# Kernel tuning notes

Hardware: AMD Instinct MI355X
Metric: run time of the kernel (lower is better)

The kernel has to match this reference:

```python
import jax, jax.numpy as jnp
import numpy as np

BN_EPS = 1e-5
L2_EPS = 1e-12


def setup_inputs() -> dict:
    key = jax.random.key(0)
    ks = jax.random.split(key, 4)
    B, C, H, W = 16, 384, 56, 56
    x = jax.random.normal(ks[0], (B, C, H, W), dtype=jnp.float32)
    w_qkv = jax.random.normal(ks[1], (3 * C, C), dtype=jnp.float32) * (1.0 / np.sqrt(C))
    b_qkv = jnp.zeros((3 * C,), dtype=jnp.float32)
    w_proj = jax.random.normal(ks[2], (C, C), dtype=jnp.float32) * (1.0 / np.sqrt(C))
    b_proj = jnp.zeros((C,), dtype=jnp.float32)
    bn_gamma = jnp.ones((C,), dtype=jnp.float32)
    bn_beta = jnp.zeros((C,), dtype=jnp.float32)
    bn_mean = jnp.zeros((C,), dtype=jnp.float32)
    bn_var = jnp.ones((C,), dtype=jnp.float32)
    temperature = jnp.ones((1,), dtype=jnp.float32)
    return {"x": x, "w_qkv": w_qkv, "b_qkv": b_qkv, "w_proj": w_proj,
            "b_proj": b_proj, "bn_gamma": bn_gamma, "bn_beta": bn_beta,
            "bn_mean": bn_mean, "bn_var": bn_var, "temperature": temperature}


def _l2norm_lastdim(t):
    # F.normalize(t, dim=-1): divide by max(||t||_2, eps)
    n = jnp.sqrt(jnp.sum(t * t, axis=-1, keepdims=True))
    return t / jnp.maximum(n, L2_EPS)


def reference(x, w_qkv, b_qkv, w_proj, b_proj, bn_gamma, bn_beta, bn_mean, bn_var, temperature):
    B, C, H, W = x.shape
    N = H * W
    # BatchNorm2d (eval mode, running stats)
    scale = bn_gamma / jnp.sqrt(bn_var + BN_EPS)          # [C]
    shift = bn_beta - bn_mean * scale                     # [C]
    xn = x * scale[None, :, None, None] + shift[None, :, None, None]
    # 1x1 conv qkv: C -> 3C, operate on flattened spatial [B, C, N]
    xn_f = xn.reshape(B, C, N)
    qkv = jnp.einsum('oc,bcn->bon', w_qkv, xn_f) + b_qkv[None, :, None]  # [B,3C,N]
    q, k, v = qkv[:, :C], qkv[:, C:2 * C], qkv[:, 2 * C:]
    q = _l2norm_lastdim(q)                                # [B,C,N]
    k = _l2norm_lastdim(k)
    # channel-transposed attention: [B,C,C]
    logits = jnp.einsum('bcn,bdn->bcd', q, k) * temperature[0]
    attn = jax.nn.softmax(logits, axis=-1)
    fused = jnp.einsum('bcd,bdn->bcn', attn, v)           # [B,C,N]
    # 1x1 proj conv + residual
    out = jnp.einsum('oc,bcn->bon', w_proj, fused) + b_proj[None, :, None]
    return x + out.reshape(B, C, H, W)
```

## Files before the change

### kernel.cpp

```cpp
#include <hip/hip_runtime.h>

#define BATCH 16
#define CCH   384
#define NSP   3136
#define NSPP  3200

typedef unsigned short u16;
typedef float  f32x4  __attribute__((ext_vector_type(4)));
typedef __bf16 bf16x8 __attribute__((ext_vector_type(8)));

__device__ __forceinline__ float bf2f(u16 u) {
  union { unsigned int i; float f; } v; v.i = ((unsigned int)u) << 16; return v.f;
}
__device__ __forceinline__ u16 f2bf(float f) {
  union { float f; unsigned int i; } v; v.f = f;
  unsigned int i = v.i;
  return (u16)((i + 0x7fffu + ((i >> 16) & 1u)) >> 16);
}
__device__ __forceinline__ float rdf(const void* p, long i, bool bf) {
  return bf ? bf2f(((const u16*)p)[i]) : ((const float*)p)[i];
}

__device__ __forceinline__ void gload_lds16(const u16* g, u16* l) {
  __builtin_amdgcn_global_load_lds(
      (const __attribute__((address_space(1))) void*)g,
      (__attribute__((address_space(3))) void*)l, 16, 0, 0);
}

__global__ void transpose_kernel(const void* __restrict__ x, u16* __restrict__ xt,
                                 u16* __restrict__ xbf, const u16* __restrict__ probe) {
  const bool bf = (probe[0] == 0x3F80u);
  __shared__ float Ls[32 * 65];
  const int t = threadIdx.x;
  const int n0 = blockIdx.x * 64, c0 = blockIdx.y * 32, b = blockIdx.z;
  if (n0 >= NSP) {
    const int n_l = t >> 2, c8 = (t & 3) * 8;
    uint4 zq = make_uint4(0, 0, 0, 0);
    *(uint4*)(xt + ((long)b * NSPP + n0 + n_l) * CCH + c0 + c8) = zq;
    return;
  }
  {
    const int c_l = t >> 3, n8 = (t & 7) * 8;
    const long src = ((long)b * CCH + c0 + c_l) * NSP + n0 + n8;
    float v[8];
    if (bf) {
      union { uint4 q; u16 e[8]; } u; u.q = *(const uint4*)((const u16*)x + src);
      #pragma unroll
      for (int i = 0; i < 8; i++) v[i] = bf2f(u.e[i]);
    } else {
      float4 a = *(const float4*)((const float*)x + src);
      float4 c = *(const float4*)((const float*)x + src + 4);
      v[0]=a.x; v[1]=a.y; v[2]=a.z; v[3]=a.w; v[4]=c.x; v[5]=c.y; v[6]=c.z; v[7]=c.w;
    }
    union { uint4 q; u16 e[8]; } ob;
    #pragma unroll
    for (int i = 0; i < 8; i++) { ob.e[i] = f2bf(v[i]); Ls[c_l * 65 + n8 + i] = v[i]; }
    *(uint4*)(xbf + src) = ob.q;
  }
  __syncthreads();
  {
    const int n_l = t >> 2, c8 = (t & 3) * 8;
    union { uint4 q; u16 e[8]; } o;
    #pragma unroll
    for (int i = 0; i < 8; i++) o.e[i] = f2bf(Ls[(c8 + i) * 65 + n_l]);
    *(uint4*)(xt + ((long)b * NSPP + n0 + n_l) * CCH + c0 + c8) = o.q;
  }
}

__global__ void prep_kernel(const void* __restrict__ w_qkv, const void* __restrict__ b_qkv,
                            const void* __restrict__ gamma, const void* __restrict__ beta,
                            const void* __restrict__ mean,  const void* __restrict__ var,
                            const void* __restrict__ b_proj, const void* __restrict__ w_proj,
                            u16* __restrict__ w_eff, float* __restrict__ b_eff,
                            float* __restrict__ bproj_f,
                            unsigned* __restrict__ w2qk, unsigned* __restrict__ wp2,
                            u16* __restrict__ wvT, float* __restrict__ szero,
                            const u16* __restrict__ probe) {
  const bool bf = (probe[0] == 0x3F80u);
  __shared__ float s_scale[CCH], s_shift[CCH];
  const int tid = threadIdx.x;
  const int o = blockIdx.x;
  if (o < 72) {
    szero[o * 256 + tid] = 0.f;
    szero[o * 256 + 128 + tid] = 0.f;
  }
  for (int c = tid; c < CCH; c += 128) {
    float g = rdf(gamma, c, bf), bt = rdf(beta, c, bf);
    float mn = rdf(mean, c, bf), vr = rdf(var, c, bf);
    float sc = g * rsqrtf(vr + 1e-5f);
    s_scale[c] = sc; s_shift[c] = bt - mn * sc;
  }
  __syncthreads();
  float part = 0.f;
  for (int c = tid; c < CCH; c += 128) {
    float w = rdf(w_qkv, (long)o * CCH + c, bf);
    u16 wv = f2bf(w * s_scale[c]);
    w_eff[(long)o * CCH + c] = wv;
    if (o < 768) w2qk[(long)o * CCH + c] = (unsigned)wv | ((unsigned)wv << 16);
    else         wvT[(long)c * CCH + (o - 768)] = wv;
    part += w * s_shift[c];
  }
  for (int off = 32; off > 0; off >>= 1) part += __shfl_down(part, off, 64);
  __shared__ float s_part[2];
  if ((tid & 63) == 0) s_part[tid >> 6] = part;
  __syncthreads();
  if (tid == 0) b_eff[o] = rdf(b_qkv, o, bf) + s_part[0] + s_part[1];
  if (o < CCH) {
    for (int c = tid; c < CCH; c += 128) {
      u16 pv = f2bf(rdf(w_proj, (long)o * CCH + c, bf));
      wp2[(long)o * CCH + c] = (unsigned)pv | ((unsigned)pv << 16);
    }
  }
  if (o == 0) {
    for (int c = tid; c < CCH; c += 128) bproj_f[c] = rdf(b_proj, c, bf);
  }
}

template<int BM, int BN, int WGM, int WGN, int OUTM, bool BIASM, bool RES,
         int NCHK, bool EPIL, bool SUMX, bool SYMM>
__launch_bounds__(256)
__global__ void gemm_nt(const u16* __restrict__ A, const u16* __restrict__ B,
                        void* __restrict__ Cv,
                        const float* __restrict__ biasm,
                        const void* __restrict__ resv,
                        int K, int lda, int ldb, int ldc,
                        long sA, long sB, long sC, long sRes,
                        int zb, int nLim, int sBM,
                        float* __restrict__ qns, const u16* __restrict__ epW,
                        float* __restrict__ sxp,
                        const u16* __restrict__ probe) {
  constexpr int WM = BM / WGM, WN = BN / WGN;
  constexpr int FM = WM / 16,  FN = WN / 16;
  constexpr int NA = BM / 32,  NB = BN / 32;
  constexpr bool BOUNCE = (OUTM == 1 || OUTM == 2) && (BM == BN) && (WGN == 2);
  constexpr int RPF = WGM * 16;
  constexpr int LBS = BN + 4;
  constexpr int SM_STAGE  = (BM + BN) * 128;
  constexpr int SM_BOUNCE = BOUNCE ? RPF * LBS * 4 : 0;
  constexpr int SM_BYTES  = SM_STAGE > SM_BOUNCE ? SM_STAGE : SM_BOUNCE;
  __shared__ __align__(16) char smem[SM_BYTES];
  u16* As = (u16*)smem;
  u16* Bs = (u16*)(smem + BM * 128);
  const bool f32io = (probe[0] != 0x3F80u);
  const int tid = threadIdx.x, wave = tid >> 6, lane = tid & 63;
  const int quad = lane >> 4, l16 = lane & 15;
  const int wm = wave / WGN, wn = wave % WGN;
  const int z = blockIdx.z;
  A += z * sA; B += z * sB;
  const long cOff = (long)(zb + z) * sC;
  const long rOff = (long)(zb + z) * sRes;

  const int gx = gridDim.x;
  const int tot = gx * gridDim.y;
  const int wg = blockIdx.y * gx + blockIdx.x;
  const int qq = tot >> 3, rr = tot & 7;
  const int xcd = wg & 7, idx = wg >> 3;
  const int nid = (xcd < rr ? xcd * (qq + 1) : rr * (qq + 1) + (xcd - rr) * qq) + idx;
  const int m0 = (nid % gx) * BM, n0 = (nid / gx) * BN;
  if (SYMM && n0 > m0) return;

  const u16* ag[NA];
  const u16* bg[NB];
  #pragma unroll
  for (int p = 0; p < NA; p++) {
    int u = tid + p * 256, r = u >> 3, k8 = u & 7;
    ag[p] = A + (long)(m0 + r) * lda + ((k8 ^ (r & 7)) << 3);
  }
  #pragma unroll
  for (int p = 0; p < NB; p++) {
    int u = tid + p * 256, r = u >> 3, k8 = u & 7;
    bg[p] = B + (long)(n0 + r) * ldb + ((k8 ^ (r & 7)) << 3);
  }

  f32x4 acc[FM][FN] = {};
  float rs[FM] = {};

  const int nt = K >> 6;
  for (int t = 0; t < nt; t++) {
    #pragma unroll
    for (int p = 0; p < NA; p++) { gload_lds16(ag[p], &As[(p * 256 + wave * 64) * 8]); ag[p] += 64; }
    #pragma unroll
    for (int p = 0; p < NB; p++) { gload_lds16(bg[p], &Bs[(p * 256 + wave * 64) * 8]); bg[p] += 64; }
    __syncthreads();

    #pragma unroll
    for (int tt = 0; tt < 2; tt++) {
      bf16x8 af[FM], bfr[FN];
      #pragma unroll
      for (int f = 0; f < FM; f++) {
        int r = wm * WM + f * 16 + l16;
        af[f] = *(const bf16x8*)&As[r * 64 + (((tt * 4 + quad) ^ (l16 & 7)) << 3)];
      }
      #pragma unroll
      for (int g = 0; g < FN; g++) {
        int r = wn * WN + g * 16 + l16;
        bfr[g] = *(const bf16x8*)&Bs[r * 64 + (((tt * 4 + quad) ^ (l16 & 7)) << 3)];
      }
      if (SUMX) {
        if (n0 == 0 && wn == 0) {
          #pragma unroll
          for (int f = 0; f < FM; f++)
            #pragma unroll
            for (int j = 0; j < 8; j++) rs[f] += (float)af[f][j];
        }
      }
      #pragma unroll
      for (int f = 0; f < FM; f++)
        #pragma unroll
        for (int g = 0; g < FN; g++)
          acc[f][g] = __builtin_amdgcn_mfma_f32_16x16x32_bf16(af[f], bfr[g], acc[f][g], 0, 0, 0);
    }
    __syncthreads();
  }

  if (SUMX) {
    if (n0 == 0 && wn == 0) {
      #pragma unroll
      for (int f = 0; f < FM; f++) {
        float r = rs[f];
        r += __shfl_xor(r, 16, 64);
        r += __shfl_xor(r, 32, 64);
        if (quad == 0) atomicAdd(sxp + (long)z * CCH + m0 + wm * WM + f * 16 + l16, r);
      }
    }
  }

  if (BOUNCE) {
    float* Lb = (float*)smem;
    #pragma unroll
    for (int f = 0; f < FM; f++) {
      #pragma unroll
      for (int g = 0; g < FN; g++)
        #pragma unroll
        for (int reg = 0; reg < 4; reg++) {
          float v = acc[f][g][reg];
          if (BIASM) v += biasm[(long)(zb + z) * sBM + m0 + wm * WM + f * 16 + quad * 4 + reg];
          Lb[(wm * 16 + quad * 4 + reg) * LBS + wn * WN + g * 16 + l16] = v;
        }
      __syncthreads();
      {
        const int tr = tid >> 3;
        const int cb = (tid & 7) * (BN / 8);
        const int mm = m0 + (tr >> 4) * WM + f * 16 + (tr & 15);
        const long rowBase = (long)mm * ldc;
        #pragma unroll
        for (int j = 0; j < BN / 32; j++) {
          const int nn = n0 + cb + j * 4;
          const bool live = (NCHK != 2) || (nn < nLim);
          if (live) {
            float4 v = *(const float4*)&Lb[tr * LBS + cb + j * 4];
            if (RES) {
              if (f32io) {
                float4 r = *(const float4*)&((const float*)resv)[rOff + rowBase + nn];
                v.x += r.x; v.y += r.y; v.z += r.z; v.w += r.w;
              } else {
                const u16* rp = (const u16*)resv + rOff + rowBase + nn;
                v.x += bf2f(rp[0]); v.y += bf2f(rp[1]); v.z += bf2f(rp[2]); v.w += bf2f(rp[3]);
              }
            }
            if (OUTM == 1 || f32io) {
              *(float4*)&((float*)Cv)[cOff + rowBase + nn] = v;
            } else {
              ushort4 o4 = { f2bf(v.x), f2bf(v.y), f2bf(v.z), f2bf(v.w) };
              *(ushort4*)((u16*)Cv + cOff + rowBase + nn) = o4;
            }
          }
        }
      }
      __syncthreads();
    }
  } else {
    #pragma unroll
    for (int f = 0; f < FM; f++) {
      #pragma unroll
      for (int reg = 0; reg < 4; reg++) {
        const int mm = m0 + wm * WM + f * 16 + quad * 4 + reg;
        float s2 = 0.f;
        #pragma unroll
        for (int g = 0; g < FN; g++) {
          int nn = n0 + wn * WN + g * 16 + l16;
          float v = acc[f][g][reg];
          if (BIASM) v += biasm[(long)(zb + z) * sBM + mm];
          long off = (long)mm * ldc + nn;
          bool live = true;
          if (NCHK == 2) live = (nn < nLim);
          if (NCHK == 3) live = (mm < nLim);
          if (RES && live) {
            long ro = rOff + off;
            v += f32io ? ((const float*)resv)[ro] : bf2f(((const u16*)resv)[ro]);
          }
          if (EPIL) s2 += v * bf2f(epW[(long)mm * CCH + nn]);
          if (OUTM == 1) {
            ((float*)Cv)[cOff + off] = v;
          } else if (OUTM == 2) {
            if (live) {
              if (f32io) ((float*)Cv)[cOff + off] = v;
              else       ((u16*)Cv)[cOff + off]   = f2bf(v);
            }
          } else if (OUTM == 4) {
            if (live) {
              u16 hi = f2bf(v);
              u16 lo = f2bf(v - bf2f(hi));
              ((unsigned*)Cv)[cOff + off] = (unsigned)hi | ((unsigned)lo << 16);
            }
          } else {
            if (live) ((u16*)Cv)[cOff + off] = f2bf(v);
          }
        }
        if (EPIL) {
          s2 += __shfl_xor(s2, 1, 16);
          s2 += __shfl_xor(s2, 2, 16);
          s2 += __shfl_xor(s2, 4, 16);
          s2 += __shfl_xor(s2, 8, 16);
          if (l16 == 0) atomicAdd(qns + (long)(zb + z) * 768 + mm, s2);
        }
      }
    }
  }
}

__global__ void mirror_ugemv_kernel(unsigned* __restrict__ Gs,
                                    const u16* __restrict__ w_eff,
                                    const float* __restrict__ sx,
                                    float* __restrict__ u) {
  const int b = blockIdx.y, bx = blockIdx.x, tid = threadIdx.x;
  if (bx < 192) {
    const int q = bx >> 6;
    const int e = (bx & 63) * 256 + tid;
    const int r = e >> 7, c = e & 127;
    const int r0 = (q == 2) ? 128 : 0;
    const int c0 = (q == 0) ? 128 : 256;
    const long base = (long)b * (CCH * CCH);
    Gs[base + (long)(r0 + r) * CCH + (c0 + c)] = Gs[base + (long)(c0 + c) * CCH + (r0 + r)];
  } else {
    const int m = (bx - 192) * 4 + (tid >> 6), l = tid & 63;
    float s = 0.f;
    for (int k = l; k < CCH; k += 64) s += bf2f(w_eff[(long)m * CCH + k]) * sx[b * CCH + k];
    for (int off = 32; off > 0; off >>= 1) s += __shfl_down(s, off, 64);
    if (l == 0) u[b * 768 + m] = s;
  }
}

__global__ void cgemv_kernel(const unsigned* __restrict__ wp2, const float* __restrict__ av,
                             const float* __restrict__ bproj, float* __restrict__ cvec) {
  const int o = blockIdx.x, b = blockIdx.y, l = threadIdx.x;
  float s = 0.f;
  for (int c = l; c < CCH; c += 64)
    s += bf2f((u16)(wp2[(long)o * CCH + c] & 0xffffu)) * av[b * CCH + c];
  for (int off = 32; off > 0; off >>= 1) s += __shfl_down(s, off, 64);
  if (l == 0) cvec[b * CCH + o] = s + bproj[o];
}

__global__ void softmax_kernel(const float* __restrict__ Lg, const float* __restrict__ qn2,
                               const float* __restrict__ u, const float* __restrict__ beff,
                               const void* __restrict__ temp,
                               u16* __restrict__ attn, float* __restrict__ av,
                               const u16* __restrict__ probe) {
  const bool bfm = (probe[0] == 0x3F80u);
  const int c = blockIdx.x, b = blockIdx.y, tid = threadIdx.x;
  const float* row = Lg + ((long)b * CCH + c) * CCH;
  const float beq = beff[c], uq = u[b * 768 + c];
  const float qn = qn2[b * 768 + c] + 2.f * beq * uq + 3136.f * beq * beq;
  const float rq = 1.f / fmaxf(sqrtf(fmaxf(qn, 0.f)), 1e-12f);
  const float T = rdf(temp, 0, bfm);
  float v[3]; float mx = -1e30f;
  #pragma unroll
  for (int j = 0; j < 3; j++) {
    int d = tid + j * 128;
    float bek = beff[384 + d], uk = u[b * 768 + 384 + d];
    float kn = qn2[b * 768 + 384 + d] + 2.f * bek * uk + 3136.f * bek * bek;
    float rd = 1.f / fmaxf(sqrtf(fmaxf(kn, 0.f)), 1e-12f);
    float lg = row[d] + uq * bek + beq * uk + 3136.f * beq * bek;
    v[j] = lg * rq * rd * T;
    mx = fmaxf(mx, v[j]);
  }
  for (int off = 32; off > 0; off >>= 1) mx = fmaxf(mx, __shfl_down(mx, off, 64));
  __shared__ float sm[2];
  if ((tid & 63) == 0) sm[tid >> 6] = mx;
  __syncthreads();
  mx = fmaxf(sm[0], sm[1]);
  float s = 0.f;
  #pragma unroll
  for (int j = 0; j < 3; j++) { v[j] = __expf(v[j] - mx); s += v[j]; }
  for (int off = 32; off > 0; off >>= 1) s += __shfl_down(s, off, 64);
  __shared__ float ss[2];
  if ((tid & 63) == 0) ss[tid >> 6] = s;
  __syncthreads();
  s = ss[0] + ss[1];
  const float inv = 1.f / s;
  float avp = 0.f;
  u16* arow = attn + ((long)b * CCH + c) * CCH;
  #pragma unroll
  for (int j = 0; j < 3; j++) {
    float p = v[j] * inv;
    arow[tid + j * 128] = f2bf(p);
    avp += p * beff[768 + tid + j * 128];
  }
  for (int off = 32; off > 0; off >>= 1) avp += __shfl_down(avp, off, 64);
  __shared__ float sa[2];
  if ((tid & 63) == 0) sa[tid >> 6] = avp;
  __syncthreads();
  if (tid == 0) av[b * CCH + c] = sa[0] + sa[1];
}

extern "C" void kernel_launch(void* const* d_in, const int* in_sizes, int n_in,
                              void* d_out, int out_size, void* d_ws, size_t ws_size,
                              hipStream_t stream) {
  const void* x      = d_in[0];
  const void* w_qkv  = d_in[1];
  const void* b_qkv  = d_in[2];
  const void* w_proj = d_in[3];
  const void* b_proj = d_in[4];
  const void* gamma  = d_in[5];
  const void* beta   = d_in[6];
  const void* mean   = d_in[7];
  const void* var    = d_in[8];
  const void* temp   = d_in[9];
  const u16* probe = (const u16*)gamma;

  const size_t SZ_XT   = (size_t)BATCH * NSPP * CCH * 2;
  const size_t SZ_XBF  = (size_t)BATCH * CCH * NSP * 2;
  const size_t SZ_WEFF = (size_t)1152 * CCH * 2;
  const size_t SZ_W2QK = (size_t)768 * CCH * 4;
  const size_t SZ_WP2  = (size_t)CCH * CCH * 4;
  const size_t SZ_WVT  = (size_t)CCH * CCH * 2;
  const size_t SZ_BEFF = (size_t)1152 * 4;
  const size_t SZ_BPRJ = (size_t)CCH * 4;
  const size_t SZ_U    = (size_t)BATCH * 768 * 4;
  const size_t SZ_AV   = (size_t)BATCH * CCH * 4;
  const size_t SZ_CV   = (size_t)BATCH * CCH * 4;
  const size_t SZ_MM   = (size_t)BATCH * CCH * CCH;

  char* ws = (char*)d_ws;
  u16*      xt    = (u16*)ws;      ws += SZ_XT;
  u16*      xbf   = (u16*)ws;      ws += SZ_XBF;
  u16*      w_eff = (u16*)ws;      ws += SZ_WEFF;
  unsigned* w2qk  = (unsigned*)ws; ws += SZ_W2QK;
  unsigned* wp2   = (unsigned*)ws; ws += SZ_WP2;
  u16*      wvT   = (u16*)ws;      ws += SZ_WVT;
  float*    b_eff = (float*)ws;    ws += SZ_BEFF;
  float*    bproj = (float*)ws;    ws += SZ_BPRJ;
  float*    sx    = (float*)ws;    ws += (size_t)BATCH * CCH * 4;
  float*    qn2   = (float*)ws;    ws += (size_t)BATCH * 768 * 4;
  float*    u     = (float*)ws;    ws += SZ_U;
  float*    av    = (float*)ws;    ws += SZ_AV;
  float*    cvec  = (float*)ws;    ws += SZ_CV;
  unsigned* Gs    = (unsigned*)ws; ws += SZ_MM * 4;
  unsigned* Ts    = (unsigned*)ws; ws += SZ_MM * 4;
  float*    Lg    = (float*)ws;    ws += SZ_MM * 4;
  u16*      attn  = (u16*)ws;      ws += SZ_MM * 2;
  unsigned* RTs   = (unsigned*)ws; ws += SZ_MM * 4;
  u16*      Mb    = (u16*)ws;      ws += SZ_MM * 2;

  const long sXB = (long)CCH * NSP;
  const long sMM = (long)CCH * CCH;
  const long sM2 = (long)CCH * 768;

  transpose_kernel<<<dim3(NSPP / 64, CCH / 32, BATCH), dim3(256), 0, stream>>>(
      x, xt, xbf, probe);
  prep_kernel<<<dim3(1152), dim3(128), 0, stream>>>(
      w_qkv, b_qkv, gamma, beta, mean, var, b_proj, w_proj,
      w_eff, b_eff, bproj, w2qk, wp2, wvT, sx, probe);

  gemm_nt<128, 128, 2, 2, 4, false, false, 0, false, true, true>
      <<<dim3(3, 3, BATCH), dim3(256), 0, stream>>>(
      xbf, xbf, Gs, nullptr, nullptr,
      NSP, NSP, NSP, CCH, sXB, sXB, sMM, 0L,
      0, 0, 0, nullptr, nullptr, sx, probe);

  mirror_ugemv_kernel<<<dim3(384, BATCH), dim3(256), 0, stream>>>(
      Gs, w_eff, sx, u);

  gemm_nt<96, 96, 2, 2, 4, false, false, 3, true, false, false>
      <<<dim3(8, 4, BATCH), dim3(256), 0, stream>>>(
      (const u16*)w2qk, (const u16*)Gs, Ts, nullptr, nullptr,
      768, 768, 768, CCH, 0L, sM2, sMM, 0L,
      0, CCH, 0, qn2, w_eff, nullptr, probe);

  gemm_nt<96, 96, 2, 2, 1, false, false, 0, false, false, false>
      <<<dim3(4, 4, BATCH), dim3(256), 0, stream>>>(
      (const u16*)Ts, (const u16*)w2qk + (long)384 * 768, Lg, nullptr, nullptr,
      768, 768, 768, CCH, sM2, 0L, sMM, 0L,
      0, 0, 0, nullptr, nullptr, nullptr, probe);

  softmax_kernel<<<dim3(CCH, BATCH), dim3(128), 0, stream>>>(
      Lg, qn2, u, b_eff, temp, attn, av, probe);

  gemm_nt<96, 96, 2, 2, 4, false, false, 0, false, false, false>
      <<<dim3(4, 4, BATCH), dim3(256), 0, stream>>>(
      wvT, attn, RTs, nullptr, nullptr,
      CCH, CCH, CCH, CCH, 0L, sMM, sMM, 0L,
      0, 0, 0, nullptr, nullptr, nullptr, probe);

  cgemv_kernel<<<dim3(CCH, BATCH), dim3(64), 0, stream>>>(wp2, av, bproj, cvec);

  gemm_nt<96, 96, 2, 2, 0, false, false, 0, false, false, false>
      <<<dim3(4, 4, BATCH), dim3(256), 0, stream>>>(
      (const u16*)wp2, (const u16*)RTs, Mb, nullptr, nullptr,
      768, 768, 768, CCH, 0L, sM2, sMM, 0L,
      0, 0, 0, nullptr, nullptr, nullptr, probe);

  gemm_nt<128, 128, 2, 2, 2, true, true, 2, false, false, false>
      <<<dim3(3, 25, BATCH), dim3(256), 0, stream>>>(
      Mb, xt, d_out, cvec, x,
      CCH, CCH, CCH, NSP, sMM, (long)NSPP * CCH, (long)CCH * NSP, (long)CCH * NSP,
      0, NSP, CCH, nullptr, nullptr, nullptr, probe);
}
```

Measured before the change: 376.2 us.

## Fuse fp32-to-bf16 conversion into Gram GEMM loads and drop symmetric skip

The Gram GEMM now reads fp32 x directly, converts it to bf16 in registers with v_cvt_pk_bf16_f32 and stores the result to LDS. This removes the separate xbf buffer write and its later re-read. The symmetric-tile skip and the mirror copy are removed, so all 9 tiles are computed, and the gemv becomes its own kernel. The transpose kernel moves to just before the final GEMM and only produces xt. In exchange, loads in the Gram GEMM go through registers instead of the async global_load_lds path, which may reduce load/compute overlap, and the lower-triangle tiles add redundant compute.

```diff
diff --git a/kernel.cpp b/kernel.cpp
--- a/kernel.cpp
+++ b/kernel.cpp
@@ -28,7 +28,7 @@
 }
 
 __global__ void transpose_kernel(const void* __restrict__ x, u16* __restrict__ xt,
-                                 u16* __restrict__ xbf, const u16* __restrict__ probe) {
+                                 const u16* __restrict__ probe) {
   const bool bf = (probe[0] == 0x3F80u);
   __shared__ float Ls[32 * 65];
   const int t = threadIdx.x;
@@ -52,10 +52,8 @@
       float4 c = *(const float4*)((const float*)x + src + 4);
       v[0]=a.x; v[1]=a.y; v[2]=a.z; v[3]=a.w; v[4]=c.x; v[5]=c.y; v[6]=c.z; v[7]=c.w;
     }
-    union { uint4 q; u16 e[8]; } ob;
     #pragma unroll
-    for (int i = 0; i < 8; i++) { ob.e[i] = f2bf(v[i]); Ls[c_l * 65 + n8 + i] = v[i]; }
-    *(uint4*)(xbf + src) = ob.q;
+    for (int i = 0; i < 8; i++) Ls[c_l * 65 + n8 + i] = v[i];
   }
   __syncthreads();
   {
@@ -117,7 +115,7 @@
 }
 
 template<int BM, int BN, int WGM, int WGN, int OUTM, bool BIASM, bool RES,
-         int NCHK, bool EPIL, bool SUMX, bool SYMM>
+         int NCHK, bool EPIL, bool SUMX, int SRC>
 __launch_bounds__(256)
 __global__ void gemm_nt(const u16* __restrict__ A, const u16* __restrict__ B,
                         void* __restrict__ Cv,
@@ -146,7 +144,10 @@
   const int quad = lane >> 4, l16 = lane & 15;
   const int wm = wave / WGN, wn = wave % WGN;
   const int z = blockIdx.z;
+  const u16* A0 = A; const u16* B0 = B;
   A += z * sA; B += z * sB;
+  const float* Af = (SRC == 1) ? ((const float*)A0 + z * sA) : nullptr;
+  const float* Bf = (SRC == 1) ? ((const float*)B0 + z * sB) : nullptr;
   const long cOff = (long)(zb + z) * sC;
   const long rOff = (long)(zb + z) * sRes;
 
@@ -157,32 +158,23 @@
   const int xcd = wg & 7, idx = wg >> 3;
   const int nid = (xcd < rr ? xcd * (qq + 1) : rr * (qq + 1) + (xcd - rr) * qq) + idx;
   const int m0 = (nid % gx) * BM, n0 = (nid / gx) * BN;
-  if (SYMM && n0 > m0) return;
-
-  const u16* ag[NA];
-  const u16* bg[NB];
+
+  long aoff[NA]; long boff[NB];
   #pragma unroll
   for (int p = 0; p < NA; p++) {
     int u = tid + p * 256, r = u >> 3, k8 = u & 7;
-    ag[p] = A + (long)(m0 + r) * lda + ((k8 ^ (r & 7)) << 3);
+    aoff[p] = (long)(m0 + r) * lda + ((k8 ^ (r & 7)) << 3);
   }
   #pragma unroll
   for (int p = 0; p < NB; p++) {
     int u = tid + p * 256, r = u >> 3, k8 = u & 7;
-    bg[p] = B + (long)(n0 + r) * ldb + ((k8 ^ (r & 7)) << 3);
+    boff[p] = (long)(n0 + r) * ldb + ((k8 ^ (r & 7)) << 3);
   }
 
   f32x4 acc[FM][FN] = {};
   float rs[FM] = {};
 
-  const int nt = K >> 6;
-  for (int t = 0; t < nt; t++) {
-    #pragma unroll
-    for (int p = 0; p < NA; p++) { gload_lds16(ag[p], &As[(p * 256 + wave * 64) * 8]); ag[p] += 64; }
-    #pragma unroll
-    for (int p = 0; p < NB; p++) { gload_lds16(bg[p], &Bs[(p * 256 + wave * 64) * 8]); bg[p] += 64; }
-    __syncthreads();
-
+  auto compute_tile = [&]() {
     #pragma unroll
     for (int tt = 0; tt < 2; tt++) {
       bf16x8 af[FM], bfr[FN];
@@ -210,7 +202,49 @@
         for (int g = 0; g < FN; g++)
           acc[f][g] = __builtin_amdgcn_mfma_f32_16x16x32_bf16(af[f], bfr[g], acc[f][g], 0, 0, 0);
     }
-    __syncthreads();
+  };
+
+  const int nt = K >> 6;
+  if (SRC == 1 && f32io) {
+    for (int t = 0; t < nt; t++) {
+      #pragma unroll
+      for (int p = 0; p < NA; p++) {
+        const float* g = Af + aoff[p] + (long)t * 64;
+        float4 lo = *(const float4*)g, hi = *(const float4*)(g + 4);
+        uint4 q;
+        asm("v_cvt_pk_bf16_f32 %0, %1, %2" : "=v"(q.x) : "v"(lo.x), "v"(lo.y));
+        asm("v_cvt_pk_bf16_f32 %0, %1, %2" : "=v"(q.y) : "v"(lo.z), "v"(lo.w));
+        asm("v_cvt_pk_bf16_f32 %0, %1, %2" : "=v"(q.z) : "v"(hi.x), "v"(hi.y));
+        asm("v_cvt_pk_bf16_f32 %0, %1, %2" : "=v"(q.w) : "v"(hi.z), "v"(hi.w));
+        *(uint4*)&As[(size_t)(tid + p * 256) * 8] = q;
+      }
+      #pragma unroll
+      for (int p = 0; p < NB; p++) {
+        const float* g = Bf + boff[p] + (long)t * 64;
+        float4 lo = *(const float4*)g, hi = *(const float4*)(g + 4);
+        uint4 q;
+        asm("v_cvt_pk_bf16_f32 %0, %1, %2" : "=v"(q.x) : "v"(lo.x), "v"(lo.y));
+        asm("v_cvt_pk_bf16_f32 %0, %1, %2" : "=v"(q.y) : "v"(lo.z), "v"(lo.w));
+        asm("v_cvt_pk_bf16_f32 %0, %1, %2" : "=v"(q.z) : "v"(hi.x), "v"(hi.y));
+        asm("v_cvt_pk_bf16_f32 %0, %1, %2" : "=v"(q.w) : "v"(hi.z), "v"(hi.w));
+        *(uint4*)&Bs[(size_t)(tid + p * 256) * 8] = q;
+      }
+      __syncthreads();
+      compute_tile();
+      __syncthreads();
+    }
+  } else {
+    for (int t = 0; t < nt; t++) {
+      #pragma unroll
+      for (int p = 0; p < NA; p++)
+        gload_lds16(A + aoff[p] + (long)t * 64, &As[(p * 256 + wave * 64) * 8]);
+      #pragma unroll
+      for (int p = 0; p < NB; p++)
+        gload_lds16(B + boff[p] + (long)t * 64, &Bs[(p * 256 + wave * 64) * 8]);
+      __syncthreads();
+      compute_tile();
+      __syncthreads();
+    }
   }
 
   if (SUMX) {
@@ -319,26 +353,14 @@
   }
 }
 
-__global__ void mirror_ugemv_kernel(unsigned* __restrict__ Gs,
-                                    const u16* __restrict__ w_eff,
-                                    const float* __restrict__ sx,
-                                    float* __restrict__ u) {
-  const int b = blockIdx.y, bx = blockIdx.x, tid = threadIdx.x;
-  if (bx < 192) {
-    const int q = bx >> 6;
-    const int e = (bx & 63) * 256 + tid;
-    const int r = e >> 7, c = e & 127;
-    const int r0 = (q == 2) ? 128 : 0;
-    const int c0 = (q == 0) ? 128 : 256;
-    const long base = (long)b * (CCH * CCH);
-    Gs[base + (long)(r0 + r) * CCH + (c0 + c)] = Gs[base + (long)(c0 + c) * CCH + (r0 + r)];
-  } else {
-    const int m = (bx - 192) * 4 + (tid >> 6), l = tid & 63;
-    float s = 0.f;
-    for (int k = l; k < CCH; k += 64) s += bf2f(w_eff[(long)m * CCH + k]) * sx[b * CCH + k];
-    for (int off = 32; off > 0; off >>= 1) s += __shfl_down(s, off, 64);
-    if (l == 0) u[b * 768 + m] = s;
-  }
+__global__ void ugemv_kernel(const u16* __restrict__ w_eff, const float* __restrict__ sx,
+                             float* __restrict__ u) {
+  const int m = blockIdx.x * 4 + (threadIdx.x >> 6), l = threadIdx.x & 63;
+  const int b = blockIdx.y;
+  float s = 0.f;
+  for (int k = l; k < CCH; k += 64) s += bf2f(w_eff[(long)m * CCH + k]) * sx[b * CCH + k];
+  for (int off = 32; off > 0; off >>= 1) s += __shfl_down(s, off, 64);
+  if (l == 0) u[b * 768 + m] = s;
 }
 
 __global__ void cgemv_kernel(const unsigned* __restrict__ wp2, const float* __restrict__ av,
@@ -419,7 +441,6 @@
   const u16* probe = (const u16*)gamma;
 
   const size_t SZ_XT   = (size_t)BATCH * NSPP * CCH * 2;
-  const size_t SZ_XBF  = (size_t)BATCH * CCH * NSP * 2;
   const size_t SZ_WEFF = (size_t)1152 * CCH * 2;
   const size_t SZ_W2QK = (size_t)768 * CCH * 4;
   const size_t SZ_WP2  = (size_t)CCH * CCH * 4;
@@ -433,7 +454,6 @@
 
   char* ws = (char*)d_ws;
   u16*      xt    = (u16*)ws;      ws += SZ_XT;
-  u16*      xbf   = (u16*)ws;      ws += SZ_XBF;
   u16*      w_eff = (u16*)ws;      ws += SZ_WEFF;
   unsigned* w2qk  = (unsigned*)ws; ws += SZ_W2QK;
   unsigned* wp2   = (unsigned*)ws; ws += SZ_WP2;
@@ -456,28 +476,25 @@
   const long sMM = (long)CCH * CCH;
   const long sM2 = (long)CCH * 768;
 
-  transpose_kernel<<<dim3(NSPP / 64, CCH / 32, BATCH), dim3(256), 0, stream>>>(
-      x, xt, xbf, probe);
   prep_kernel<<<dim3(1152), dim3(128), 0, stream>>>(
       w_qkv, b_qkv, gamma, beta, mean, var, b_proj, w_proj,
       w_eff, b_eff, bproj, w2qk, wp2, wvT, sx, probe);
 
-  gemm_nt<128, 128, 2, 2, 4, false, false, 0, false, true, true>
+  gemm_nt<128, 128, 2, 2, 4, false, false, 0, false, true, 1>
       <<<dim3(3, 3, BATCH), dim3(256), 0, stream>>>(
-      xbf, xbf, Gs, nullptr, nullptr,
+      (const u16*)x, (const u16*)x, Gs, nullptr, nullptr,
       NSP, NSP, NSP, CCH, sXB, sXB, sMM, 0L,
       0, 0, 0, nullptr, nullptr, sx, probe);
 
-  mirror_ugemv_kernel<<<dim3(384, BATCH), dim3(256), 0, stream>>>(
-      Gs, w_eff, sx, u);
-
-  gemm_nt<96, 96, 2, 2, 4, false, false, 3, true, false, false>
+  ugemv_kernel<<<dim3(192, BATCH), dim3(256), 0, stream>>>(w_eff, sx, u);
+
+  gemm_nt<96, 96, 2, 2, 4, false, false, 3, true, false, 0>
       <<<dim3(8, 4, BATCH), dim3(256), 0, stream>>>(
       (const u16*)w2qk, (const u16*)Gs, Ts, nullptr, nullptr,
       768, 768, 768, CCH, 0L, sM2, sMM, 0L,
       0, CCH, 0, qn2, w_eff, nullptr, probe);
 
-  gemm_nt<96, 96, 2, 2, 1, false, false, 0, false, false, false>
+  gemm_nt<96, 96, 2, 2, 1, false, false, 0, false, false, 0>
       <<<dim3(4, 4, BATCH), dim3(256), 0, stream>>>(
       (const u16*)Ts, (const u16*)w2qk + (long)384 * 768, Lg, nullptr, nullptr,
       768, 768, 768, CCH, sM2, 0L, sMM, 0L,
@@ -486,7 +503,7 @@
   softmax_kernel<<<dim3(CCH, BATCH), dim3(128), 0, stream>>>(
       Lg, qn2, u, b_eff, temp, attn, av, probe);
 
-  gemm_nt<96, 96, 2, 2, 4, false, false, 0, false, false, false>
+  gemm_nt<96, 96, 2, 2, 4, false, false, 0, false, false, 0>
       <<<dim3(4, 4, BATCH), dim3(256), 0, stream>>>(
       wvT, attn, RTs, nullptr, nullptr,
       CCH, CCH, CCH, CCH, 0L, sMM, sMM, 0L,
@@ -494,13 +511,16 @@
 
   cgemv_kernel<<<dim3(CCH, BATCH), dim3(64), 0, stream>>>(wp2, av, bproj, cvec);
 
-  gemm_nt<96, 96, 2, 2, 0, false, false, 0, false, false, false>
+  gemm_nt<96, 96, 2, 2, 0, false, false, 0, false, false, 0>
       <<<dim3(4, 4, BATCH), dim3(256), 0, stream>>>(
       (const u16*)wp2, (const u16*)RTs, Mb, nullptr, nullptr,
       768, 768, 768, CCH, 0L, sM2, sMM, 0L,
       0, 0, 0, nullptr, nullptr, nullptr, probe);
 
-  gemm_nt<128, 128, 2, 2, 2, true, true, 2, false, false, false>
+  transpose_kernel<<<dim3(NSPP / 64, CCH / 32, BATCH), dim3(256), 0, stream>>>(
+      x, xt, probe);
+
+  gemm_nt<128, 128, 2, 2, 2, true, true, 2, false, false, 0>
       <<<dim3(3, 25, BATCH), dim3(256), 0, stream>>>(
       Mb, xt, d_out, cvec, x,
       CCH, CCH, CCH, NSP, sMM, (long)NSPP * CCH, (long)CCH * NSP, (long)CCH * NSP,
```

Result: slower. 383.9 us (+2.1%).
